# Kernel tuning notes

Measured on AMD Instinct MI355X. Metric: run time of the kernel, lower is better.

The kernel has to match this reference:

```python
import jax, jax.numpy as jnp
import numpy as np

B, S, E, H = 8, 2048, 1024, 64  # batch, seq (== block_size), emb_size, head_size


def setup_inputs() -> dict:
    key = jax.random.key(0)
    ks = jax.random.split(key, 7)
    s = 1.0 / np.sqrt(E)  # ~ torch Linear default init scale
    return {
        "x": jax.random.normal(ks[0], (B, S, E), dtype=jnp.float32),
        "Wk": jax.random.uniform(ks[1], (H, E), jnp.float32, -s, s),
        "bk": jax.random.uniform(ks[2], (H,), jnp.float32, -s, s),
        "Wq": jax.random.uniform(ks[3], (H, E), jnp.float32, -s, s),
        "bq": jax.random.uniform(ks[4], (H,), jnp.float32, -s, s),
        "Wv": jax.random.uniform(ks[5], (H, E), jnp.float32, -s, s),
        "bv": jax.random.uniform(ks[6], (H,), jnp.float32, -s, s),
    }


def reference(x, Wk, bk, Wq, bq, Wv, bv):
    # Linear projections (torch Linear: y = x @ W.T + b)
    xk = jnp.einsum('bse,he->bsh', x, Wk) + bk  # [B,S,H]
    xq = jnp.einsum('bse,he->bsh', x, Wq) + bq
    xv = jnp.einsum('bse,he->bsh', x, Wv) + bv
    # raw scores q @ k^T  -> [B,S,S]
    wei = jnp.einsum('bqh,bkh->bqk', xq, xk)
    # causal mask (encoder=True branch in source; tril==0 -> -inf)
    causal = jnp.tril(jnp.ones((x.shape[1], x.shape[1]), dtype=bool))
    wei = jnp.where(causal, wei, -jnp.inf)
    # NOTE: source divides by head_size**(-0.5), i.e. MULTIPLIES by sqrt(head_size)
    scale = jnp.asarray(Wk.shape[0], jnp.float32) ** 0.5
    wei = jax.nn.softmax(wei * scale, axis=-1)
    return jnp.einsum('bqk,bkh->bqh', wei, xv)
```

## Files before the change

kernel.cpp:

```cpp
#include <hip/hip_runtime.h>

typedef _Float16 f16;
typedef _Float16 f16x8 __attribute__((ext_vector_type(8)));
typedef _Float16 f16x4 __attribute__((ext_vector_type(4)));
typedef float f32x4 __attribute__((ext_vector_type(4)));

#define MFMA16(a, b, c) __builtin_amdgcn_mfma_f32_16x16x32_f16(a, b, c, 0, 0, 0)

constexpr int Bn = 8, Sn = 2048, En = 1024, Hn = 64;
constexpr int Mn = Bn * Sn;
constexpr float QSCALE = 11.5415603f;
constexpr float THR = 11.5f;

__device__ __forceinline__ void gload_lds16(const void* g, void* lds) {
    __builtin_amdgcn_global_load_lds(
        (const __attribute__((address_space(1))) void*)g,
        (__attribute__((address_space(3))) void*)lds, 16, 0, 0);
}
__device__ __forceinline__ void wait_vm4() {
    asm volatile("s_waitcnt vmcnt(4)" ::: "memory");
    __builtin_amdgcn_sched_barrier(0);
}
__device__ __forceinline__ void wait_vm0() {
    asm volatile("s_waitcnt vmcnt(0)" ::: "memory");
    __builtin_amdgcn_sched_barrier(0);
}
__device__ __forceinline__ void barrier_raw() {
    __builtin_amdgcn_s_barrier();
    __builtin_amdgcn_sched_barrier(0);
}

__global__ __launch_bounds__(256) void convw_kernel(
    const float* __restrict__ Wq, const float* __restrict__ Wk,
    const float* __restrict__ Wv, f16* __restrict__ Wc)
{
    const int h = blockIdx.x * 256 + threadIdx.x;
    const int kt = h / 1536;
    const int rem = h - kt * 1536;
    const int rr = rem >> 3;
    const int c = rem & 7;
    const int set = rr >> 6;
    const float* src = (set == 0 ? Wq : (set == 1 ? Wk : Wv))
                       + (size_t)(rr & 63) * En + kt * 64 + c * 8;
    float4 v0 = *reinterpret_cast<const float4*>(src);
    float4 v1 = *reinterpret_cast<const float4*>(src + 4);
    f16x8 o = {(f16)v0.x, (f16)v0.y, (f16)v0.z, (f16)v0.w,
               (f16)v1.x, (f16)v1.y, (f16)v1.z, (f16)v1.w};
    const int cs = c ^ (rr & 7);
    *reinterpret_cast<f16x8*>(Wc + (size_t)kt * 12288 + rr * 64 + cs * 8) = o;
}

__global__ __launch_bounds__(512) void proj_kernel(
    const float* __restrict__ x, const f16* __restrict__ Wc,
    const float* __restrict__ bq, const float* __restrict__ bk,
    const float* __restrict__ bv,
    f16* __restrict__ qws, f16* __restrict__ kws, f16* __restrict__ vtws)
{
    __shared__ __align__(16) char ldsb[2 * 32768];
    const int tid = threadIdx.x;
    const int w = tid >> 6, l = tid & 63;
    const int l15 = l & 15, lhi = l >> 4;
    const int rt = w & 1, nh = w >> 1;
    const int Mbase = blockIdx.x * 32;

    f32x4 acc[3];
#pragma unroll
    for (int i = 0; i < 3; ++i) acc[i] = (f32x4){0.f, 0.f, 0.f, 0.f};

    const int xr_s = w * 4 + (l >> 4);
    const int xc_s = (l & 15) ^ (xr_s & 7);

#define WSTAGE(buf, kb)                                                       \
    {                                                                         \
        const f16* wt_ = Wc + (size_t)(kb) * 12288;                           \
        _Pragma("unroll")                                                     \
        for (int r_ = 0; r_ < 3; ++r_)                                        \
            gload_lds16(wt_ + r_ * 4096 + w * 512 + l * 8,                    \
                        ldsb + (buf) * 32768 + r_ * 8192 + w * 1024);         \
    }

#define XSTAGE(buf, kb)                                                       \
    {                                                                         \
        const float* xs_ = x + (size_t)(Mbase + xr_s) * En + (kb) * 64        \
                           + xc_s * 4;                                        \
        gload_lds16(xs_, ldsb + (buf) * 32768 + 24576 + w * 1024);            \
    }

#define COMPUTE(buf)                                                          \
    {                                                                         \
        const int xrow_ = rt * 16 + l15;                                      \
        const char* xb_ = ldsb + (buf) * 32768 + 24576 + xrow_ * 256;         \
        f16x8 a_[2];                                                          \
        _Pragma("unroll")                                                     \
        for (int kc_ = 0; kc_ < 2; ++kc_) {                                   \
            const int c0_ = kc_ * 8 + lhi * 2;                                \
            float4 lo_ = *reinterpret_cast<const float4*>(                    \
                xb_ + ((c0_ ^ (l15 & 7)) * 16));                              \
            float4 hi_ = *reinterpret_cast<const float4*>(                    \
                xb_ + (((c0_ + 1) ^ (l15 & 7)) * 16));                        \
            a_[kc_] = (f16x8){(f16)lo_.x, (f16)lo_.y, (f16)lo_.z, (f16)lo_.w, \
                              (f16)hi_.x, (f16)hi_.y, (f16)hi_.z, (f16)hi_.w};\
        }                                                                     \
        _Pragma("unroll")                                                     \
        for (int i_ = 0; i_ < 3; ++i_) {                                      \
            const int row16_ = (nh * 3 + i_) * 16 + l15;                      \
            _Pragma("unroll")                                                 \
            for (int kc_ = 0; kc_ < 2; ++kc_) {                               \
                const int addr_ = (buf) * 32768 + row16_ * 128                \
                    + ((kc_ * 64 + lhi * 16) ^ ((l15 & 7) << 4));             \
                f16x8 b_ = *reinterpret_cast<const f16x8*>(ldsb + addr_);     \
                acc[i_] = MFMA16(a_[kc_], b_, acc[i_]);                       \
            }                                                                 \
        }                                                                     \
    }

    WSTAGE(0, 0);
    XSTAGE(0, 0);
#pragma unroll
    for (int i = 0; i < 16; ++i) {
        const int cur = i & 1;
        if (i < 15) {
            WSTAGE(cur ^ 1, i + 1);
            XSTAGE(cur ^ 1, i + 1);
            wait_vm4();
        } else {
            wait_vm0();
        }
        barrier_raw();
        COMPUTE(cur);
        barrier_raw();
    }
#undef WSTAGE
#undef XSTAGE
#undef COMPUTE

    const int batch = Mbase >> 11;
    const int r0 = Mbase + rt * 16 + lhi * 4;
#pragma unroll
    for (int i = 0; i < 3; ++i) {
        const int nt = nh * 3 + i;
        const int set = nt >> 2;
        const int h = (nt & 3) * 16 + l15;
        const float bias = (set == 0 ? bq : (set == 1 ? bk : bv))[h];
        if (set == 0) {
#pragma unroll
            for (int r = 0; r < 4; ++r)
                qws[(size_t)(r0 + r) * Hn + h] =
                    (f16)((acc[i][r] + bias) * QSCALE);
        } else if (set == 1) {
#pragma unroll
            for (int r = 0; r < 4; ++r)
                kws[(size_t)(r0 + r) * Hn + h] = (f16)(acc[i][r] + bias);
        } else {
            const int s0v = r0 & (Sn - 1);
            const int sp = (s0v & ~31) + ((s0v & 12) << 1)
                         + ((s0v & 16) ? 4 : 0);
            f16x4 hv = {(f16)(acc[i][0] + bias), (f16)(acc[i][1] + bias),
                        (f16)(acc[i][2] + bias), (f16)(acc[i][3] + bias)};
            *reinterpret_cast<f16x4*>(
                &vtws[(size_t)batch * Hn * Sn + (size_t)h * Sn + sp]) = hv;
        }
    }
}

__global__ __launch_bounds__(256, 3) void attn_kernel(
    const f16* __restrict__ qws, const f16* __restrict__ kws,
    const f16* __restrict__ vtws, float* __restrict__ out,
    float* __restrict__ slots)
{
    const int tid = threadIdx.x;
    const int w = tid >> 6, l = tid & 63;
    const int l15 = l & 15, lhi = l >> 4;

    const int L = blockIdx.x * 4 + w;
    const int u = (int)(((unsigned)L * 997u) % 2304u);
    const int b = u / 288;
    const int t = u - b * 288;
    int k = 0;
#pragma unroll
    for (int gg = 1; gg < 8; ++gg)
        if (t >= 4 * gg * (gg + 1)) k = gg;
    const int rem = t - 4 * k * (k + 1);
    const int jq = rem / (k + 1);
    const int c = rem - jq * (k + 1);
    const int J = 8 * k + jq;

    const int qbase = J * 32;
    const int nkt = J + 1;
    const int ts = c * 8;
    const int te = (ts + 8 < nkt) ? ts + 8 : nkt;
    const bool hasDiag = (te == nkt);
    const int nfull = te - (hasDiag ? 1 : 0);

    const f16* qb = qws + (size_t)b * Sn * Hn;
    const f16* kb = kws + (size_t)b * Sn * Hn;
    const f16* vtb = vtws + (size_t)b * Hn * Sn;

    f16x8 qf[2][2];
#pragma unroll
    for (int rs = 0; rs < 2; ++rs)
#pragma unroll
        for (int kc = 0; kc < 2; ++kc)
            qf[rs][kc] = *reinterpret_cast<const f16x8*>(
                &qb[(size_t)(qbase + rs * 16 + l15) * Hn + kc * 32 + lhi * 8]);

    f32x4 O[2][4];
#pragma unroll
    for (int rs = 0; rs < 2; ++rs)
#pragma unroll
        for (int nt = 0; nt < 4; ++nt) O[rs][nt] = (f32x4){0.f, 0.f, 0.f, 0.f};
    float m1[2] = {-1e30f, -1e30f}, l1[2] = {0.f, 0.f};

#define ATTN_ITER(KT, MASKED)                                                 \
    {                                                                         \
        const int kbase = (KT) * 32;                                          \
        f16x8 kf[2][2];                                                       \
        _Pragma("unroll") for (int nt = 0; nt < 2; ++nt)                      \
        _Pragma("unroll") for (int kc = 0; kc < 2; ++kc)                      \
            kf[nt][kc] = *reinterpret_cast<const f16x8*>(                     \
                &kb[(size_t)(kbase + nt * 16 + l15) * Hn + kc * 32            \
                    + lhi * 8]);                                              \
        f32x4 Sv[2][2];                                                       \
        _Pragma("unroll") for (int rs = 0; rs < 2; ++rs)                      \
        _Pragma("unroll") for (int nt = 0; nt < 2; ++nt) {                    \
            f32x4 sa = (f32x4){0.f, 0.f, 0.f, 0.f};                           \
            sa = MFMA16(kf[nt][0], qf[rs][0], sa);                            \
            sa = MFMA16(kf[nt][1], qf[rs][1], sa);                            \
            Sv[rs][nt] = sa;                                                  \
        }                                                                     \
        float tv[2][2][4];                                                    \
        float mx[2];                                                          \
        _Pragma("unroll") for (int rs = 0; rs < 2; ++rs) {                    \
            _Pragma("unroll") for (int nt = 0; nt < 2; ++nt)                  \
            _Pragma("unroll") for (int r = 0; r < 4; ++r) {                   \
                float v = Sv[rs][nt][r];                                      \
                if (MASKED) {                                                 \
                    const int key_ = nt * 16 + lhi * 4 + r;                   \
                    const int qq_ = rs * 16 + l15;                            \
                    v = (key_ <= qq_) ? v : -1e30f;                           \
                }                                                             \
                tv[rs][nt][r] = v;                                            \
            }                                                                 \
            float a0 = fmaxf(fmaxf(tv[rs][0][0], tv[rs][0][1]),               \
                             fmaxf(tv[rs][0][2], tv[rs][0][3]));              \
            float a1 = fmaxf(fmaxf(tv[rs][1][0], tv[rs][1][1]),               \
                             fmaxf(tv[rs][1][2], tv[rs][1][3]));              \
            float m_ = fmaxf(a0, a1);                                         \
            m_ = fmaxf(m_, __shfl_xor(m_, 16));                               \
            m_ = fmaxf(m_, __shfl_xor(m_, 32));                               \
            mx[rs] = m_;                                                      \
        }                                                                     \
        const int need = (mx[0] > m1[0] + THR) || (mx[1] > m1[1] + THR);      \
        if (__any(need)) {                                                    \
            _Pragma("unroll") for (int rs = 0; rs < 2; ++rs) {                \
                const float mn = fmaxf(m1[rs], mx[rs]);                       \
                const float al = exp2f(m1[rs] - mn);                          \
                l1[rs] *= al;                                                 \
                _Pragma("unroll") for (int nt = 0; nt < 4; ++nt)              \
                _Pragma("unroll") for (int r = 0; r < 4; ++r)                 \
                    O[rs][nt][r] *= al;                                       \
                m1[rs] = mn;                                                  \
            }                                                                 \
        }                                                                     \
        f16x8 pa[2];                                                          \
        _Pragma("unroll") for (int rs = 0; rs < 2; ++rs) {                    \
            float p_[8];                                                      \
            float s_ = 0.f;                                                   \
            _Pragma("unroll") for (int nt = 0; nt < 2; ++nt)                  \
            _Pragma("unroll") for (int r = 0; r < 4; ++r) {                   \
                const float e_ = exp2f(tv[rs][nt][r] - m1[rs]);               \
                p_[nt * 4 + r] = e_;                                          \
                s_ += e_;                                                     \
            }                                                                 \
            s_ += __shfl_xor(s_, 16);                                         \
            s_ += __shfl_xor(s_, 32);                                         \
            l1[rs] += s_;                                                     \
            pa[rs] = (f16x8){(f16)p_[0], (f16)p_[1], (f16)p_[2], (f16)p_[3],  \
                             (f16)p_[4], (f16)p_[5], (f16)p_[6], (f16)p_[7]}; \
        }                                                                     \
        _Pragma("unroll") for (int nt = 0; nt < 4; ++nt) {                    \
            f16x8 vf = *reinterpret_cast<const f16x8*>(                       \
                &vtb[(size_t)(nt * 16 + l15) * Sn + kbase + lhi * 8]);        \
            O[0][nt] = MFMA16(vf, pa[0], O[0][nt]);                           \
            O[1][nt] = MFMA16(vf, pa[1], O[1][nt]);                           \
        }                                                                     \
    }

    for (int kt = ts; kt < nfull; ++kt) ATTN_ITER(kt, false);
    if (hasDiag) ATTN_ITER(J, true);
#undef ATTN_ITER

    if (J < 8) {
#pragma unroll
        for (int rs = 0; rs < 2; ++rs) {
            const float inv = 1.0f / l1[rs];
            const size_t ro = ((size_t)b * Sn + qbase + rs * 16 + l15) * Hn;
#pragma unroll
            for (int nt = 0; nt < 4; ++nt) {
                float4 o = {O[rs][nt][0] * inv, O[rs][nt][1] * inv,
                            O[rs][nt][2] * inv, O[rs][nt][3] * inv};
                *reinterpret_cast<float4*>(&out[ro + nt * 16 + lhi * 4]) = o;
            }
        }
    } else {
        float* sl = slots + (size_t)(b * 280 + 4 * k * (k + 1) - 8
                                     + jq * (k + 1) + c) * 1088;
        f16* so = reinterpret_cast<f16*>(sl + 64);
#pragma unroll
        for (int rs = 0; rs < 2; ++rs) {
            const int row = rs * 16 + l15;
            const float inv = 1.0f / l1[rs];
            if (lhi == 0) { sl[row] = m1[rs]; sl[32 + row] = l1[rs]; }
#pragma unroll
            for (int nt = 0; nt < 4; ++nt) {
                f16x4 hv = {(f16)(O[rs][nt][0] * inv), (f16)(O[rs][nt][1] * inv),
                            (f16)(O[rs][nt][2] * inv), (f16)(O[rs][nt][3] * inv)};
                *reinterpret_cast<f16x4*>(
                    &so[row * 64 + nt * 16 + lhi * 4]) = hv;
            }
        }
    }
}

__global__ __launch_bounds__(256) void comb_kernel(
    const float* __restrict__ slots, float* __restrict__ out)
{
    const int id = blockIdx.x;
    const int b = id / 56, jj = id - b * 56;
    const int J = 8 + jj;
    const int k = J >> 3;
    const int nch = k + 1;
    const float* base = slots + (size_t)(b * 280 + 4 * k * (k + 1) - 8
                                         + (J - 8 * k) * (k + 1)) * 1088;
    const int tid = threadIdx.x;
    const int row = tid >> 3;
    const int h0 = (tid & 7) * 8;

    float mg = -1e30f;
    for (int cc = 0; cc < nch; ++cc)
        mg = fmaxf(mg, base[cc * 1088 + row]);
    float den = 0.f;
    float num[8] = {0.f, 0.f, 0.f, 0.f, 0.f, 0.f, 0.f, 0.f};
    for (int cc = 0; cc < nch; ++cc) {
        const float* sl = base + cc * 1088;
        const float wgt = sl[32 + row] * exp2f(sl[row] - mg);
        den += wgt;
        const f16* so = reinterpret_cast<const f16*>(sl + 64);
        f16x8 ov = *reinterpret_cast<const f16x8*>(&so[row * 64 + h0]);
#pragma unroll
        for (int i = 0; i < 8; ++i) num[i] += (float)ov[i] * wgt;
    }
    const float inv = 1.0f / den;
    const size_t ro = ((size_t)b * Sn + J * 32 + row) * Hn + h0;
    float4 o0 = {num[0] * inv, num[1] * inv, num[2] * inv, num[3] * inv};
    float4 o1 = {num[4] * inv, num[5] * inv, num[6] * inv, num[7] * inv};
    *reinterpret_cast<float4*>(&out[ro]) = o0;
    *reinterpret_cast<float4*>(&out[ro + 4]) = o1;
}

extern "C" void kernel_launch(void* const* d_in, const int* in_sizes, int n_in,
                              void* d_out, int out_size, void* d_ws, size_t ws_size,
                              hipStream_t stream) {
    const float* x  = (const float*)d_in[0];
    const float* Wk = (const float*)d_in[1];
    const float* bk = (const float*)d_in[2];
    const float* Wq = (const float*)d_in[3];
    const float* bq = (const float*)d_in[4];
    const float* Wv = (const float*)d_in[5];
    const float* bv = (const float*)d_in[6];

    f16* qws  = (f16*)d_ws;
    f16* kws  = qws + (size_t)Mn * Hn;
    f16* vtws = kws + (size_t)Mn * Hn;
    f16* Wc   = vtws + (size_t)Mn * Hn;
    float* slots = (float*)(Wc + 196608);

    convw_kernel<<<96, 256, 0, stream>>>(Wq, Wk, Wv, Wc);
    proj_kernel<<<512, 512, 0, stream>>>(x, Wc, bq, bk, bv, qws, kws, vtws);
    attn_kernel<<<576, 256, 0, stream>>>(qws, kws, vtws, (float*)d_out, slots);
    comb_kernel<<<448, 256, 0, stream>>>(slots, (float*)d_out);
}
```

Baseline: 61.09 us.

## Halve attention split-K chunk size and use packed fp16 conversions

The attention split-K decomposition now uses chunks of 4 key tiles instead of 8, which doubles the number of waves (1088 blocks) and changes the slot indexing and combine kernel grid to match. The aim is better load balance and occupancy across CUs and a shorter critical path per wave. In exchange, more partial results are written to and read back from the slot buffer, so the combine pass does more work. Separately, float-to-fp16 conversions are replaced with packed round-toward-zero cvt_pkrtz intrinsics, which cut instruction count but change the rounding mode.

New measurement: 66.43 us. 1.09x slower.

```diff
diff --git a/kernel.cpp b/kernel.cpp
--- a/kernel.cpp
+++ b/kernel.cpp
@@ -3,6 +3,7 @@
 typedef _Float16 f16;
 typedef _Float16 f16x8 __attribute__((ext_vector_type(8)));
 typedef _Float16 f16x4 __attribute__((ext_vector_type(4)));
+typedef __fp16 fp16x2 __attribute__((ext_vector_type(2)));
 typedef float f32x4 __attribute__((ext_vector_type(4)));
 
 #define MFMA16(a, b, c) __builtin_amdgcn_mfma_f32_16x16x32_f16(a, b, c, 0, 0, 0)
@@ -28,6 +29,14 @@
 __device__ __forceinline__ void barrier_raw() {
     __builtin_amdgcn_s_barrier();
     __builtin_amdgcn_sched_barrier(0);
+}
+__device__ __forceinline__ f16x8 cvt8(float4 lo, float4 hi) {
+    union { f16x8 v; fp16x2 h[4]; } u;
+    u.h[0] = __builtin_amdgcn_cvt_pkrtz(lo.x, lo.y);
+    u.h[1] = __builtin_amdgcn_cvt_pkrtz(lo.z, lo.w);
+    u.h[2] = __builtin_amdgcn_cvt_pkrtz(hi.x, hi.y);
+    u.h[3] = __builtin_amdgcn_cvt_pkrtz(hi.z, hi.w);
+    return u.v;
 }
 
 __global__ __launch_bounds__(256) void convw_kernel(
@@ -44,8 +53,7 @@
                        + (size_t)(rr & 63) * En + kt * 64 + c * 8;
     float4 v0 = *reinterpret_cast<const float4*>(src);
     float4 v1 = *reinterpret_cast<const float4*>(src + 4);
-    f16x8 o = {(f16)v0.x, (f16)v0.y, (f16)v0.z, (f16)v0.w,
-               (f16)v1.x, (f16)v1.y, (f16)v1.z, (f16)v1.w};
+    f16x8 o = cvt8(v0, v1);
     const int cs = c ^ (rr & 7);
     *reinterpret_cast<f16x8*>(Wc + (size_t)kt * 12288 + rr * 64 + cs * 8) = o;
 }
@@ -98,8 +106,7 @@
                 xb_ + ((c0_ ^ (l15 & 7)) * 16));                              \
             float4 hi_ = *reinterpret_cast<const float4*>(                    \
                 xb_ + (((c0_ + 1) ^ (l15 & 7)) * 16));                        \
-            a_[kc_] = (f16x8){(f16)lo_.x, (f16)lo_.y, (f16)lo_.z, (f16)lo_.w, \
-                              (f16)hi_.x, (f16)hi_.y, (f16)hi_.z, (f16)hi_.w};\
+            a_[kc_] = cvt8(lo_, hi_);                                         \
         }                                                                     \
         _Pragma("unroll")                                                     \
         for (int i_ = 0; i_ < 3; ++i_) {                                      \
@@ -173,22 +180,22 @@
     const int l15 = l & 15, lhi = l >> 4;
 
     const int L = blockIdx.x * 4 + w;
-    const int u = (int)(((unsigned)L * 997u) % 2304u);
-    const int b = u / 288;
-    const int t = u - b * 288;
-    int k = 0;
-#pragma unroll
-    for (int gg = 1; gg < 8; ++gg)
-        if (t >= 4 * gg * (gg + 1)) k = gg;
-    const int rem = t - 4 * k * (k + 1);
-    const int jq = rem / (k + 1);
-    const int c = rem - jq * (k + 1);
-    const int J = 8 * k + jq;
+    const int u = (int)(((unsigned)L * 997u) % 4352u);
+    const int b = u / 544;
+    const int t = u - b * 544;
+    int g = 0;
+#pragma unroll
+    for (int gg = 1; gg < 16; ++gg)
+        if (t >= 2 * gg * (gg + 1)) g = gg;
+    const int rem = t - 2 * g * (g + 1);
+    const int jq = rem / (g + 1);
+    const int c = rem - jq * (g + 1);
+    const int J = 4 * g + jq;
 
     const int qbase = J * 32;
     const int nkt = J + 1;
-    const int ts = c * 8;
-    const int te = (ts + 8 < nkt) ? ts + 8 : nkt;
+    const int ts = c * 4;
+    const int te = (ts + 4 < nkt) ? ts + 4 : nkt;
     const bool hasDiag = (te == nkt);
     const int nfull = te - (hasDiag ? 1 : 0);
 
@@ -275,8 +282,8 @@
             s_ += __shfl_xor(s_, 16);                                         \
             s_ += __shfl_xor(s_, 32);                                         \
             l1[rs] += s_;                                                     \
-            pa[rs] = (f16x8){(f16)p_[0], (f16)p_[1], (f16)p_[2], (f16)p_[3],  \
-                             (f16)p_[4], (f16)p_[5], (f16)p_[6], (f16)p_[7]}; \
+            pa[rs] = cvt8((float4){p_[0], p_[1], p_[2], p_[3]},               \
+                          (float4){p_[4], p_[5], p_[6], p_[7]});              \
         }                                                                     \
         _Pragma("unroll") for (int nt = 0; nt < 4; ++nt) {                    \
             f16x8 vf = *reinterpret_cast<const f16x8*>(                       \
@@ -290,7 +297,7 @@
     if (hasDiag) ATTN_ITER(J, true);
 #undef ATTN_ITER
 
-    if (J < 8) {
+    if (J < 4) {
 #pragma unroll
         for (int rs = 0; rs < 2; ++rs) {
             const float inv = 1.0f / l1[rs];
@@ -303,8 +310,8 @@
             }
         }
     } else {
-        float* sl = slots + (size_t)(b * 280 + 4 * k * (k + 1) - 8
-                                     + jq * (k + 1) + c) * 1088;
+        float* sl = slots + (size_t)(b * 540 + 2 * g * (g + 1) - 4
+                                     + jq * (g + 1) + c) * 1088;
         f16* so = reinterpret_cast<f16*>(sl + 64);
 #pragma unroll
         for (int rs = 0; rs < 2; ++rs) {
@@ -326,12 +333,12 @@
     const float* __restrict__ slots, float* __restrict__ out)
 {
     const int id = blockIdx.x;
-    const int b = id / 56, jj = id - b * 56;
-    const int J = 8 + jj;
-    const int k = J >> 3;
-    const int nch = k + 1;
-    const float* base = slots + (size_t)(b * 280 + 4 * k * (k + 1) - 8
-                                         + (J - 8 * k) * (k + 1)) * 1088;
+    const int b = id / 60, jj = id - b * 60;
+    const int J = 4 + jj;
+    const int g = J >> 2;
+    const int nch = g + 1;
+    const float* base = slots + (size_t)(b * 540 + 2 * g * (g + 1) - 4
+                                         + (J - 4 * g) * (g + 1)) * 1088;
     const int tid = threadIdx.x;
     const int row = tid >> 3;
     const int h0 = (tid & 7) * 8;
@@ -377,6 +384,6 @@
 
     convw_kernel<<<96, 256, 0, stream>>>(Wq, Wk, Wv, Wc);
     proj_kernel<<<512, 512, 0, stream>>>(x, Wc, bq, bk, bv, qws, kws, vtws);
-    attn_kernel<<<576, 256, 0, stream>>>(qws, kws, vtws, (float*)d_out, slots);
-    comb_kernel<<<448, 256, 0, stream>>>(slots, (float*)d_out);
-}
+    attn_kernel<<<1088, 256, 0, stream>>>(qws, kws, vtws, (float*)d_out, slots);
+    comb_kernel<<<480, 256, 0, stream>>>(slots, (float*)d_out);
+}
```
